# Optimization experiments

Measured on AMD Instinct MI355X. Metric: run time of the kernel, lower is better.

The kernel has to match this reference:

```python
import jax, jax.numpy as jnp
import numpy as np

N_NODES = 50000
N_EDGES = 600000
D_IN = 128
D_HID = 128


def setup_inputs() -> dict:
    key = jax.random.key(0)
    ks = jax.random.split(key, 12)
    edge_index = jax.random.randint(ks[0], (2, N_EDGES), 0, N_NODES)
    x = jax.random.normal(ks[1], (N_NODES, D_IN), dtype=jnp.float32)
    shuffled_x = jax.random.normal(ks[2], (N_NODES, D_IN), dtype=jnp.float32)
    # DIMPLayer params: linear transform applied after neighbor aggregation
    sc = 1.0 / np.sqrt(D_IN)
    W0 = jax.random.uniform(ks[3], (D_IN, D_HID), jnp.float32, -sc, sc)
    b0 = jnp.zeros((D_HID,), jnp.float32)
    W1 = jax.random.uniform(ks[4], (D_HID, D_HID), jnp.float32, -sc, sc)
    b1 = jnp.zeros((D_HID,), jnp.float32)
    W2 = jax.random.uniform(ks[5], (D_HID, D_HID), jnp.float32, -sc, sc)
    b2 = jnp.zeros((D_HID,), jnp.float32)
    # Bilinear discriminator weight
    Wd = jax.random.uniform(ks[6], (D_HID, D_HID), jnp.float32, -sc, sc)
    return {"edge_index": edge_index, "x": x, "shuffled_x": shuffled_x,
            "W0": W0, "b0": b0, "W1": W1, "b1": b1, "W2": W2, "b2": b2,
            "Wd": Wd}


def reference(edge_index, x, shuffled_x, W0, b0, W1, b1, W2, b2, Wd):
    src, dst = edge_index[0], edge_index[1]
    n = x.shape[0]

    def dimp_layer(h, W, b):
        # gather source-node features along edges, scatter-add into destinations
        agg = jax.ops.segment_sum(h[src], dst, num_segments=n)  # [N, d]
        return jax.nn.relu(agg @ W + b)

    params = [(W0, b0), (W1, b1), (W2, b2)]

    def encode(feat):
        h = feat
        for W, b in params:
            h = dimp_layer(h, W, b)
        return h

    h = encode(x)                    # [N, D_HID]
    s = jnp.mean(h, axis=0)          # [D_HID] graph summary
    shuffled_h = encode(shuffled_x)  # [N, D_HID]

    # Bilinear discriminator: logit_i = h_i^T Wd s
    ws = Wd @ s                      # [D_HID]
    d_h = h @ ws                     # [N]
    d_shuffled_h = shuffled_h @ ws   # [N]
    return jnp.concatenate((d_h, d_shuffled_h), axis=0)  # [2N]
```

## Files before the change

### kernel.cpp

```cpp
#include <hip/hip_runtime.h>

#define D 128

typedef short bf16x8 __attribute__((ext_vector_type(8)));
typedef float f32x4 __attribute__((ext_vector_type(4)));

static __device__ __forceinline__ unsigned short f2bf(float f) {
    unsigned int u = __float_as_uint(f);
    u = u + 0x7FFFu + ((u >> 16) & 1u);
    return (unsigned short)(u >> 16);
}
static __device__ __forceinline__ float bf2f(unsigned short h) {
    return __uint_as_float(((unsigned int)h) << 16);
}


__global__ __launch_bounds__(256) void count_kernel(const int* __restrict__ dst,
        int* __restrict__ counts, int E) {
    int e = blockIdx.x * 256 + threadIdx.x;
    if (e < E) atomicAdd(&counts[dst[e]], 1);
}

__global__ __launch_bounds__(256) void scan_reduce(const int* __restrict__ counts,
        int* __restrict__ bsum, int n) {
    int b = blockIdx.x, t = threadIdx.x;
    int base = b * 1024 + t * 4;
    int s = 0;
    #pragma unroll
    for (int i = 0; i < 4; ++i) {
        int idx = base + i;
        if (idx < n) s += counts[idx];
    }
    __shared__ int sd[256];
    sd[t] = s;
    __syncthreads();
    #pragma unroll
    for (int off = 128; off > 0; off >>= 1) {
        if (t < off) sd[t] += sd[t + off];
        __syncthreads();
    }
    if (t == 0) bsum[b] = sd[0];
}

__global__ __launch_bounds__(64) void scan_tops(const int* __restrict__ bsum,
        int* __restrict__ bofs, int* __restrict__ row_ptr_end, int B) {
    int t = threadIdx.x;
    int v = (t < B) ? bsum[t] : 0;
    int inc = v;
    #pragma unroll
    for (int off = 1; off < 64; off <<= 1) {
        int u = __shfl_up(inc, off);
        if (t >= off) inc += u;
    }
    if (t < B) bofs[t] = inc - v;
    if (t == 63) *row_ptr_end = inc;
}

__global__ __launch_bounds__(256) void scan_final(const int* __restrict__ counts,
        const int* __restrict__ bofs, int* __restrict__ row_ptr,
        int* __restrict__ cursor, int n) {
    int b = blockIdx.x, t = threadIdx.x;
    int base = b * 1024 + t * 4;
    int v[4];
    int s = 0;
    #pragma unroll
    for (int i = 0; i < 4; ++i) {
        int idx = base + i;
        v[i] = (idx < n) ? counts[idx] : 0;
        s += v[i];
    }
    __shared__ int sd[256];
    sd[t] = s;
    __syncthreads();
    #pragma unroll
    for (int off = 1; off < 256; off <<= 1) {
        int u = (t >= off) ? sd[t - off] : 0;
        __syncthreads();
        sd[t] += u;
        __syncthreads();
    }
    int excl = bofs[b] + sd[t] - s;
    #pragma unroll
    for (int i = 0; i < 4; ++i) {
        int idx = base + i;
        if (idx < n) {
            row_ptr[idx] = excl;
            cursor[idx] = excl;
            excl += v[i];
        }
    }
}

__global__ __launch_bounds__(256) void fill_kernel(const int* __restrict__ src,
        const int* __restrict__ dst, int* __restrict__ cursor,
        int* __restrict__ src_sorted, int E) {
    int e = blockIdx.x * 256 + threadIdx.x;
    if (e < E) {
        int p = atomicAdd(&cursor[dst[e]], 1);
        src_sorted[p] = src[e];
    }
}


__global__ __launch_bounds__(256) void cvt_kernel(const float* __restrict__ in,
        unsigned short* __restrict__ out, int n4) {
    int i = blockIdx.x * 256 + threadIdx.x;
    if (i < n4) {
        float4 v = ((const float4*)in)[i];
        ushort4 o;
        o.x = f2bf(v.x); o.y = f2bf(v.y); o.z = f2bf(v.z); o.w = f2bf(v.w);
        ((ushort4*)out)[i] = o;
    }
}


__global__ __launch_bounds__(256) void pack_w(const float* __restrict__ W,
        unsigned short* __restrict__ Wp) {
    int t = blockIdx.x * 256 + threadIdx.x;
    if (t >= 2048) return;
    int lane = t & 63;
    int ct = (t >> 6) & 7;
    int s = t >> 9;
    int n = ct * 16 + (lane & 15);
    int k0 = s * 32 + (lane >> 4) * 8;
    unsigned short hi[8], lo[8];
    #pragma unroll
    for (int j = 0; j < 8; ++j) {
        float f = W[(size_t)(k0 + j) * 128 + n];
        unsigned short h = f2bf(f);
        hi[j] = h;
        lo[j] = f2bf(f - bf2f(h));
    }
    size_t bh = ((size_t)((s * 8 + ct) * 2 + 0) * 64 + lane) * 8;
    size_t bl = ((size_t)((s * 8 + ct) * 2 + 1) * 64 + lane) * 8;
    #pragma unroll
    for (int j = 0; j < 8; ++j) { Wp[bh + j] = hi[j]; Wp[bl + j] = lo[j]; }
}


__global__ __launch_bounds__(256) void agg_gemm(const unsigned short* __restrict__ Hin,
        const int* __restrict__ row_ptr, const int* __restrict__ src_sorted,
        const unsigned short* __restrict__ Wp, const float* __restrict__ bias,
        unsigned short* __restrict__ Hout, int N, int NT,
        float* __restrict__ mean_out, int Nmean, float inv_n) {
    __shared__ float Af[64][129];
    __shared__ float red[4][128];
    int tid = threadIdx.x;
    int bm = blockIdx.x * 64;

    {
        int lane = tid & 15;
        int ng   = tid >> 4;
        const uint4* h4 = (const uint4*)Hin;

        auto addv = [](float* a, uint4 v) {
            a[0] += __uint_as_float(v.x << 16);
            a[1] += __uint_as_float(v.x & 0xFFFF0000u);
            a[2] += __uint_as_float(v.y << 16);
            a[3] += __uint_as_float(v.y & 0xFFFF0000u);
            a[4] += __uint_as_float(v.z << 16);
            a[5] += __uint_as_float(v.z & 0xFFFF0000u);
            a[6] += __uint_as_float(v.w << 16);
            a[7] += __uint_as_float(v.w & 0xFFFF0000u);
        };

        #pragma unroll
        for (int g = 0; g < 4; ++g) {
            int local = g * 16 + ng;
            int node = bm + local; if (node >= NT) node = NT - 1;
            int base = (node < N) ? 0 : N;
            int rp = node - base;
            int beg = row_ptr[rp], end = row_ptr[rp + 1];

            float acc[8];
            #pragma unroll
            for (int i = 0; i < 8; ++i) acc[i] = 0.f;

            int j = beg;
            for (; j + 3 < end; j += 4) {
                int s0 = src_sorted[j]     + base;
                int s1 = src_sorted[j + 1] + base;
                int s2 = src_sorted[j + 2] + base;
                int s3 = src_sorted[j + 3] + base;
                uint4 v0 = h4[(size_t)s0 * 16 + lane];
                uint4 v1 = h4[(size_t)s1 * 16 + lane];
                uint4 v2 = h4[(size_t)s2 * 16 + lane];
                uint4 v3 = h4[(size_t)s3 * 16 + lane];
                addv(acc, v0); addv(acc, v1); addv(acc, v2); addv(acc, v3);
            }
            for (; j < end; ++j) {
                int s0 = src_sorted[j] + base;
                addv(acc, h4[(size_t)s0 * 16 + lane]);
            }
            #pragma unroll
            for (int i = 0; i < 8; ++i) Af[local][lane * 8 + i] = acc[i];
        }
    }
    __syncthreads();

    int w = tid >> 6, l = tid & 63;
    int fr = l & 15;
    int kg = l >> 4;
    int m0 = bm + w * 16;

    f32x4 acc[8];
    #pragma unroll
    for (int ct = 0; ct < 8; ++ct) acc[ct] = (f32x4){0.f, 0.f, 0.f, 0.f};

    const float* arow = &Af[w * 16 + fr][0];
    const uint4* wp4 = (const uint4*)Wp;

    for (int s = 0; s < 4; ++s) {
        bf16x8 a_hi, a_lo;
        #pragma unroll
        for (int jj = 0; jj < 8; ++jj) {
            float f = arow[s * 32 + kg * 8 + jj];
            unsigned short h = f2bf(f);
            a_hi[jj] = (short)h;
            a_lo[jj] = (short)f2bf(f - bf2f(h));
        }
        #pragma unroll
        for (int ct = 0; ct < 8; ++ct) {
            uint4 bhu = wp4[(size_t)((s * 8 + ct) * 2 + 0) * 64 + l];
            uint4 blu = wp4[(size_t)((s * 8 + ct) * 2 + 1) * 64 + l];
            bf16x8 b_hi, b_lo;
            *(uint4*)&b_hi = bhu;
            *(uint4*)&b_lo = blu;
            acc[ct] = __builtin_amdgcn_mfma_f32_16x16x32_bf16(a_hi, b_hi, acc[ct], 0, 0, 0);
            acc[ct] = __builtin_amdgcn_mfma_f32_16x16x32_bf16(a_lo, b_hi, acc[ct], 0, 0, 0);
            acc[ct] = __builtin_amdgcn_mfma_f32_16x16x32_bf16(a_hi, b_lo, acc[ct], 0, 0, 0);
        }
    }

    float colsum[8];
    #pragma unroll
    for (int ct = 0; ct < 8; ++ct) {
        int col = ct * 16 + fr;
        float b = bias[col];
        float cs = 0.f;
        #pragma unroll
        for (int r = 0; r < 4; ++r) {
            int m = m0 + kg * 4 + r;
            float v = fmaxf(acc[ct][r] + b, 0.f);
            if (m < NT) Hout[(size_t)m * 128 + col] = f2bf(v);
            if (m < Nmean) cs += v;
        }
        colsum[ct] = cs;
    }

    if (mean_out) {
        #pragma unroll
        for (int ct = 0; ct < 8; ++ct) {
            float v = colsum[ct];
            v += __shfl_xor(v, 16);
            v += __shfl_xor(v, 32);
            if (l < 16) red[w][ct * 16 + l] = v;
        }
        __syncthreads();
        if (tid < 128) {
            float s = red[0][tid] + red[1][tid] + red[2][tid] + red[3][tid];
            if (s != 0.f) atomicAdd(&mean_out[tid], s * inv_n);
        }
    }
}


__global__ __launch_bounds__(128) void wd_kernel(const float* __restrict__ Wd,
        const float* __restrict__ s, float* __restrict__ wsv) {
    __shared__ float sl[128];
    int i = threadIdx.x;
    sl[i] = s[i];
    __syncthreads();
    float acc = 0.f;
    for (int j = 0; j < 128; ++j) acc += Wd[(size_t)i * 128 + j] * sl[j];
    wsv[i] = acc;
}


__global__ __launch_bounds__(256) void disc_kernel(const unsigned short* __restrict__ h,
        const float* __restrict__ wsv, float* __restrict__ out, int n) {
    int wave = threadIdx.x >> 6, lane = threadIdx.x & 63;
    int node = blockIdx.x * 4 + wave;
    if (node >= n) return;
    unsigned int hv = ((const unsigned int*)h)[(size_t)node * 64 + lane];
    float2 wv = *(const float2*)&wsv[lane * 2];
    float lo = __uint_as_float(hv << 16);
    float hi = __uint_as_float(hv & 0xFFFF0000u);
    float acc = lo * wv.x + hi * wv.y;
    #pragma unroll
    for (int off = 32; off > 0; off >>= 1) acc += __shfl_down(acc, off);
    if (lane == 0) out[node] = acc;
}


extern "C" void kernel_launch(void* const* d_in, const int* in_sizes, int n_in,
                              void* d_out, int out_size, void* d_ws, size_t ws_size,
                              hipStream_t stream) {
    const int* edge_index = (const int*)d_in[0];
    const float* x  = (const float*)d_in[1];
    const float* sx = (const float*)d_in[2];
    const float* W0 = (const float*)d_in[3];
    const float* b0 = (const float*)d_in[4];
    const float* W1 = (const float*)d_in[5];
    const float* b1 = (const float*)d_in[6];
    const float* W2 = (const float*)d_in[7];
    const float* b2 = (const float*)d_in[8];
    const float* Wd = (const float*)d_in[9];
    float* out = (float*)d_out;

    const int E = in_sizes[0] / 2;
    const int N = in_sizes[1] / D;
    const int* src = edge_index;
    const int* dst = edge_index + E;
    const float inv_n = 1.0f / (float)N;

    char* wsp = (char*)d_ws;
    size_t off = 0;
    auto alloc = [&](size_t bytes) -> void* {
        void* p = wsp + off;
        off += (bytes + 511) & ~(size_t)511;
        return p;
    };
    int* counts     = (int*)alloc((size_t)N * 4);
    int* row_ptr    = (int*)alloc((size_t)(N + 1) * 4);
    int* cursor     = (int*)alloc((size_t)N * 4);
    int* src_sorted = (int*)alloc((size_t)E * 4);
    int* bsum       = (int*)alloc(64 * 4);
    int* bofs       = (int*)alloc(64 * 4);
    float* svec     = (float*)alloc(D * 4);
    float* wsv      = (float*)alloc(D * 4);
    unsigned short* wp0 = (unsigned short*)alloc((size_t)D * D * 2 * 2);
    unsigned short* wp1 = (unsigned short*)alloc((size_t)D * D * 2 * 2);
    unsigned short* wp2 = (unsigned short*)alloc((size_t)D * D * 2 * 2);

    size_t fixed = off;
    size_t need_batched = fixed + 2 * ((size_t)2 * N * D * 2 + 512);
    bool batched = ws_size >= need_batched;
    int NB = batched ? 2 * N : N;

    unsigned short* hbufA = (unsigned short*)alloc((size_t)NB * D * 2);
    unsigned short* hbufB = (unsigned short*)alloc((size_t)NB * D * 2);

    hipMemsetAsync(counts, 0, (size_t)N * 4, stream);
    hipMemsetAsync(svec, 0, D * 4, stream);

    pack_w<<<8, 256, 0, stream>>>(W0, wp0);
    pack_w<<<8, 256, 0, stream>>>(W1, wp1);
    pack_w<<<8, 256, 0, stream>>>(W2, wp2);

    int eblocks = (E + 255) / 256;
    int sblocks = (N + 1023) / 1024;
    count_kernel<<<eblocks, 256, 0, stream>>>(dst, counts, E);
    scan_reduce<<<sblocks, 256, 0, stream>>>(counts, bsum, N);
    scan_tops<<<1, 64, 0, stream>>>(bsum, bofs, row_ptr + N, sblocks);
    scan_final<<<sblocks, 256, 0, stream>>>(counts, bofs, row_ptr, cursor, N);
    fill_kernel<<<eblocks, 256, 0, stream>>>(src, dst, cursor, src_sorted, E);

    int n4 = N * D / 4;
    int cblocks = (n4 + 255) / 256;
    int gblocks = (NB + 63) / 64;

    if (batched) {
        cvt_kernel<<<cblocks, 256, 0, stream>>>(x, hbufA, n4);
        cvt_kernel<<<cblocks, 256, 0, stream>>>(sx, hbufA + (size_t)N * D, n4);
        agg_gemm<<<gblocks, 256, 0, stream>>>(hbufA, row_ptr, src_sorted, wp0, b0,
                                              hbufB, N, NB, nullptr, 0, 0.f);
        agg_gemm<<<gblocks, 256, 0, stream>>>(hbufB, row_ptr, src_sorted, wp1, b1,
                                              hbufA, N, NB, nullptr, 0, 0.f);
        agg_gemm<<<gblocks, 256, 0, stream>>>(hbufA, row_ptr, src_sorted, wp2, b2,
                                              hbufB, N, NB, svec, N, inv_n);
        wd_kernel<<<1, 128, 0, stream>>>(Wd, svec, wsv);
        disc_kernel<<<(NB + 3) / 4, 256, 0, stream>>>(hbufB, wsv, out, NB);
    } else {
        auto encode = [&](const float* input, float* mean_out) {
            cvt_kernel<<<cblocks, 256, 0, stream>>>(input, hbufA, n4);
            agg_gemm<<<gblocks, 256, 0, stream>>>(hbufA, row_ptr, src_sorted, wp0, b0,
                                                  hbufB, N, NB, nullptr, 0, 0.f);
            agg_gemm<<<gblocks, 256, 0, stream>>>(hbufB, row_ptr, src_sorted, wp1, b1,
                                                  hbufA, N, NB, nullptr, 0, 0.f);
            agg_gemm<<<gblocks, 256, 0, stream>>>(hbufA, row_ptr, src_sorted, wp2, b2,
                                                  hbufB, N, NB, mean_out, mean_out ? N : 0, inv_n);
        };
        encode(x, svec);
        wd_kernel<<<1, 128, 0, stream>>>(Wd, svec, wsv);
        disc_kernel<<<(NB + 3) / 4, 256, 0, stream>>>(hbufB, wsv, out, NB);
        encode(sx, nullptr);
        disc_kernel<<<(NB + 3) / 4, 256, 0, stream>>>(hbufB, wsv, out + N, NB);
    }
}
```

Measured before the change: 339.5 us.

## Sort nodes by in-degree for load-balanced aggregation and add dual accumulators

Builds a degree histogram and a counting-sort permutation so each aggregation block handles nodes of similar in-degree, and in batched mode pairs each node with its shuffled twin. The goal is to reduce intra-wave divergence from uneven neighbor counts. The gather loop is also unrolled to eight loads with two accumulator sets to raise memory-level parallelism. In exchange, output rows are written in scattered permuted order, the locality of consecutive node ids is lost, and three small kernels are added.

Result: slower. 700.5 us (+106.3%).

```diff
diff --git a/kernel.cpp b/kernel.cpp
--- a/kernel.cpp
+++ b/kernel.cpp
@@ -98,6 +98,40 @@
     if (e < E) {
         int p = atomicAdd(&cursor[dst[e]], 1);
         src_sorted[p] = src[e];
+    }
+}
+
+
+__global__ __launch_bounds__(256) void hist_kernel(const int* __restrict__ counts,
+        int* __restrict__ hist, int n) {
+    int i = blockIdx.x * 256 + threadIdx.x;
+    if (i < n) atomicAdd(&hist[min(counts[i], 255)], 1);
+}
+
+__global__ __launch_bounds__(256) void scan_hist(const int* __restrict__ hist,
+        int* __restrict__ binofs) {
+    __shared__ int sd[256];
+    int t = threadIdx.x;
+    int v = hist[t];
+    sd[t] = v;
+    __syncthreads();
+    #pragma unroll
+    for (int off = 1; off < 256; off <<= 1) {
+        int u = (t >= off) ? sd[t - off] : 0;
+        __syncthreads();
+        sd[t] += u;
+        __syncthreads();
+    }
+    binofs[t] = sd[t] - v;
+}
+
+__global__ __launch_bounds__(256) void scatter_perm(const int* __restrict__ counts,
+        int* __restrict__ binofs, int* __restrict__ perm, int n) {
+    int i = blockIdx.x * 256 + threadIdx.x;
+    if (i < n) {
+        int b = min(counts[i], 255);
+        int p = atomicAdd(&binofs[b], 1);
+        perm[p] = i;
     }
 }
 
@@ -140,13 +174,21 @@
 
 __global__ __launch_bounds__(256) void agg_gemm(const unsigned short* __restrict__ Hin,
         const int* __restrict__ row_ptr, const int* __restrict__ src_sorted,
+        const int* __restrict__ perm,
         const unsigned short* __restrict__ Wp, const float* __restrict__ bias,
-        unsigned short* __restrict__ Hout, int N, int NT,
+        unsigned short* __restrict__ Hout, int N, int NT, int paired,
         float* __restrict__ mean_out, int Nmean, float inv_n) {
     __shared__ float Af[64][129];
     __shared__ float red[4][128];
+    __shared__ int nid[64];
     int tid = threadIdx.x;
     int bm = blockIdx.x * 64;
+
+    if (tid < 64) {
+        int s = bm + tid; if (s >= NT) s = NT - 1;
+        nid[tid] = paired ? (perm[s >> 1] + (s & 1) * N) : perm[s];
+    }
+    __syncthreads();
 
     {
         int lane = tid & 15;
@@ -167,33 +209,48 @@
         #pragma unroll
         for (int g = 0; g < 4; ++g) {
             int local = g * 16 + ng;
-            int node = bm + local; if (node >= NT) node = NT - 1;
-            int base = (node < N) ? 0 : N;
+            int node = nid[local];
+            int base = (node >= N) ? N : 0;
             int rp = node - base;
             int beg = row_ptr[rp], end = row_ptr[rp + 1];
 
-            float acc[8];
+            float acc0[8], acc1[8];
             #pragma unroll
-            for (int i = 0; i < 8; ++i) acc[i] = 0.f;
+            for (int i = 0; i < 8; ++i) { acc0[i] = 0.f; acc1[i] = 0.f; }
 
             int j = beg;
-            for (; j + 3 < end; j += 4) {
-                int s0 = src_sorted[j]     + base;
-                int s1 = src_sorted[j + 1] + base;
-                int s2 = src_sorted[j + 2] + base;
-                int s3 = src_sorted[j + 3] + base;
-                uint4 v0 = h4[(size_t)s0 * 16 + lane];
-                uint4 v1 = h4[(size_t)s1 * 16 + lane];
-                uint4 v2 = h4[(size_t)s2 * 16 + lane];
-                uint4 v3 = h4[(size_t)s3 * 16 + lane];
-                addv(acc, v0); addv(acc, v1); addv(acc, v2); addv(acc, v3);
+            for (; j + 7 < end; j += 8) {
+                uint4 v0 = h4[(size_t)(src_sorted[j    ] + base) * 16 + lane];
+                uint4 v1 = h4[(size_t)(src_sorted[j + 1] + base) * 16 + lane];
+                uint4 v2 = h4[(size_t)(src_sorted[j + 2] + base) * 16 + lane];
+                uint4 v3 = h4[(size_t)(src_sorted[j + 3] + base) * 16 + lane];
+                uint4 v4 = h4[(size_t)(src_sorted[j + 4] + base) * 16 + lane];
+                uint4 v5 = h4[(size_t)(src_sorted[j + 5] + base) * 16 + lane];
+                uint4 v6 = h4[(size_t)(src_sorted[j + 6] + base) * 16 + lane];
+                uint4 v7 = h4[(size_t)(src_sorted[j + 7] + base) * 16 + lane];
+                addv(acc0, v0); addv(acc1, v1); addv(acc0, v2); addv(acc1, v3);
+                addv(acc0, v4); addv(acc1, v5); addv(acc0, v6); addv(acc1, v7);
             }
-            for (; j < end; ++j) {
-                int s0 = src_sorted[j] + base;
-                addv(acc, h4[(size_t)s0 * 16 + lane]);
+            if (j + 3 < end) {
+                uint4 v0 = h4[(size_t)(src_sorted[j    ] + base) * 16 + lane];
+                uint4 v1 = h4[(size_t)(src_sorted[j + 1] + base) * 16 + lane];
+                uint4 v2 = h4[(size_t)(src_sorted[j + 2] + base) * 16 + lane];
+                uint4 v3 = h4[(size_t)(src_sorted[j + 3] + base) * 16 + lane];
+                addv(acc0, v0); addv(acc1, v1); addv(acc0, v2); addv(acc1, v3);
+                j += 4;
+            }
+            if (j + 1 < end) {
+                uint4 v0 = h4[(size_t)(src_sorted[j    ] + base) * 16 + lane];
+                uint4 v1 = h4[(size_t)(src_sorted[j + 1] + base) * 16 + lane];
+                addv(acc0, v0); addv(acc1, v1);
+                j += 2;
+            }
+            if (j < end) {
+                uint4 v0 = h4[(size_t)(src_sorted[j] + base) * 16 + lane];
+                addv(acc0, v0);
             }
             #pragma unroll
-            for (int i = 0; i < 8; ++i) Af[local][lane * 8 + i] = acc[i];
+            for (int i = 0; i < 8; ++i) Af[local][lane * 8 + i] = acc0[i] + acc1[i];
         }
     }
     __syncthreads();
@@ -201,7 +258,6 @@
     int w = tid >> 6, l = tid & 63;
     int fr = l & 15;
     int kg = l >> 4;
-    int m0 = bm + w * 16;
 
     f32x4 acc[8];
     #pragma unroll
@@ -240,10 +296,13 @@
         float cs = 0.f;
         #pragma unroll
         for (int r = 0; r < 4; ++r) {
-            int m = m0 + kg * 4 + r;
+            int lm = w * 16 + kg * 4 + r;
             float v = fmaxf(acc[ct][r] + b, 0.f);
-            if (m < NT) Hout[(size_t)m * 128 + col] = f2bf(v);
-            if (m < Nmean) cs += v;
+            if (bm + lm < NT) {
+                int node = nid[lm];
+                Hout[(size_t)node * 128 + col] = f2bf(v);
+                if (node < Nmean) cs += v;
+            }
         }
         colsum[ct] = cs;
     }
@@ -327,6 +386,9 @@
     int* src_sorted = (int*)alloc((size_t)E * 4);
     int* bsum       = (int*)alloc(64 * 4);
     int* bofs       = (int*)alloc(64 * 4);
+    int* hist       = (int*)alloc(256 * 4);
+    int* binofs     = (int*)alloc(256 * 4);
+    int* perm       = (int*)alloc((size_t)N * 4);
     float* svec     = (float*)alloc(D * 4);
     float* wsv      = (float*)alloc(D * 4);
     unsigned short* wp0 = (unsigned short*)alloc((size_t)D * D * 2 * 2);
@@ -337,11 +399,13 @@
     size_t need_batched = fixed + 2 * ((size_t)2 * N * D * 2 + 512);
     bool batched = ws_size >= need_batched;
     int NB = batched ? 2 * N : N;
+    int paired = batched ? 1 : 0;
 
     unsigned short* hbufA = (unsigned short*)alloc((size_t)NB * D * 2);
     unsigned short* hbufB = (unsigned short*)alloc((size_t)NB * D * 2);
 
     hipMemsetAsync(counts, 0, (size_t)N * 4, stream);
+    hipMemsetAsync(hist, 0, 256 * 4, stream);
     hipMemsetAsync(svec, 0, D * 4, stream);
 
     pack_w<<<8, 256, 0, stream>>>(W0, wp0);
@@ -349,12 +413,16 @@
     pack_w<<<8, 256, 0, stream>>>(W2, wp2);
 
     int eblocks = (E + 255) / 256;
+    int nblocks = (N + 255) / 256;
     int sblocks = (N + 1023) / 1024;
     count_kernel<<<eblocks, 256, 0, stream>>>(dst, counts, E);
     scan_reduce<<<sblocks, 256, 0, stream>>>(counts, bsum, N);
     scan_tops<<<1, 64, 0, stream>>>(bsum, bofs, row_ptr + N, sblocks);
     scan_final<<<sblocks, 256, 0, stream>>>(counts, bofs, row_ptr, cursor, N);
     fill_kernel<<<eblocks, 256, 0, stream>>>(src, dst, cursor, src_sorted, E);
+    hist_kernel<<<nblocks, 256, 0, stream>>>(counts, hist, N);
+    scan_hist<<<1, 256, 0, stream>>>(hist, binofs);
+    scatter_perm<<<nblocks, 256, 0, stream>>>(counts, binofs, perm, N);
 
     int n4 = N * D / 4;
     int cblocks = (n4 + 255) / 256;
@@ -363,23 +431,23 @@
     if (batched) {
         cvt_kernel<<<cblocks, 256, 0, stream>>>(x, hbufA, n4);
         cvt_kernel<<<cblocks, 256, 0, stream>>>(sx, hbufA + (size_t)N * D, n4);
-        agg_gemm<<<gblocks, 256, 0, stream>>>(hbufA, row_ptr, src_sorted, wp0, b0,
-                                              hbufB, N, NB, nullptr, 0, 0.f);
-        agg_gemm<<<gblocks, 256, 0, stream>>>(hbufB, row_ptr, src_sorted, wp1, b1,
-                                              hbufA, N, NB, nullptr, 0, 0.f);
-        agg_gemm<<<gblocks, 256, 0, stream>>>(hbufA, row_ptr, src_sorted, wp2, b2,
-                                              hbufB, N, NB, svec, N, inv_n);
+        agg_gemm<<<gblocks, 256, 0, stream>>>(hbufA, row_ptr, src_sorted, perm, wp0, b0,
+                                              hbufB, N, NB, paired, nullptr, 0, 0.f);
+        agg_gemm<<<gblocks, 256, 0, stream>>>(hbufB, row_ptr, src_sorted, perm, wp1, b1,
+                                              hbufA, N, NB, paired, nullptr, 0, 0.f);
+        agg_gemm<<<gblocks, 256, 0, stream>>>(hbufA, row_ptr, src_sorted, perm, wp2, b2,
+                                              hbufB, N, NB, paired, svec, N, inv_n);
         wd_kernel<<<1, 128, 0, stream>>>(Wd, svec, wsv);
         disc_kernel<<<(NB + 3) / 4, 256, 0, stream>>>(hbufB, wsv, out, NB);
     } else {
         auto encode = [&](const float* input, float* mean_out) {
             cvt_kernel<<<cblocks, 256, 0, stream>>>(input, hbufA, n4);
-            agg_gemm<<<gblocks, 256, 0, stream>>>(hbufA, row_ptr, src_sorted, wp0, b0,
-                                                  hbufB, N, NB, nullptr, 0, 0.f);
-            agg_gemm<<<gblocks, 256, 0, stream>>>(hbufB, row_ptr, src_sorted, wp1, b1,
-                                                  hbufA, N, NB, nullptr, 0, 0.f);
-            agg_gemm<<<gblocks, 256, 0, stream>>>(hbufA, row_ptr, src_sorted, wp2, b2,
-                                                  hbufB, N, NB, mean_out, mean_out ? N : 0, inv_n);
+            agg_gemm<<<gblocks, 256, 0, stream>>>(hbufA, row_ptr, src_sorted, perm, wp0, b0,
+                                                  hbufB, N, NB, paired, nullptr, 0, 0.f);
+            agg_gemm<<<gblocks, 256, 0, stream>>>(hbufB, row_ptr, src_sorted, perm, wp1, b1,
+                                                  hbufA, N, NB, paired, nullptr, 0, 0.f);
+            agg_gemm<<<gblocks, 256, 0, stream>>>(hbufA, row_ptr, src_sorted, perm, wp2, b2,
+                                                  hbufB, N, NB, paired, mean_out, mean_out ? N : 0, inv_n);
         };
         encode(x, svec);
         wd_kernel<<<1, 128, 0, stream>>>(Wd, svec, wsv);
```
